# Kernel tuning notes

Hardware: AMD Instinct MI355X
Metric: run time of the kernel (lower is better)

Reference implementation:

```python
import jax, jax.numpy as jnp
import numpy as np

INPUT_DIM, ATTN_DIM, OUTPUT_DIM = 1024, 1024, 1024
B, LQ, LKV = 4, 2048, 2048


def setup_inputs() -> dict:
    key = jax.random.key(0)
    ks = jax.random.split(key, 10)
    s = 1.0 / np.sqrt(INPUT_DIM)
    return {
        "primary": jax.random.normal(ks[0], (B, LQ, INPUT_DIM), jnp.float32),
        "context_sequence": jax.random.normal(ks[1], (B, LKV, INPUT_DIM), jnp.float32),
        "mask": jax.random.randint(ks[2], (B, LQ, LKV), 0, 2).astype(jnp.float32),
        "Wq": jax.random.uniform(ks[3], (INPUT_DIM, ATTN_DIM), jnp.float32, -s, s),
        "bq": jax.random.uniform(ks[4], (ATTN_DIM,), jnp.float32, -s, s),
        "Wk": jax.random.uniform(ks[5], (INPUT_DIM, ATTN_DIM), jnp.float32, -s, s),
        "bk": jax.random.uniform(ks[6], (ATTN_DIM,), jnp.float32, -s, s),
        "Wv": jax.random.uniform(ks[7], (INPUT_DIM, OUTPUT_DIM), jnp.float32, -s, s),
        "bv": jax.random.uniform(ks[8], (OUTPUT_DIM,), jnp.float32, -s, s),
    }


def reference(primary, context_sequence, mask, Wq, bq, Wk, bk, Wv, bv):
    q = primary @ Wq + bq                      # [B, Lq, attn_dim]
    k = context_sequence @ Wk + bk             # [B, Lkv, attn_dim]
    v = context_sequence @ Wv + bv             # [B, Lkv, output_dim]
    score = jnp.einsum('bqd,bkd->bqk', q, k) / jnp.sqrt(jnp.float32(ATTN_DIM))
    score = score + mask * (-1e9)
    attn = jax.nn.softmax(score, axis=-1)
    return jnp.einsum('bqk,bkd->bqd', attn, v)  # [B, Lq, output_dim]
```

## Files before the change

### kernel.cpp

```cpp
#include <hip/hip_runtime.h>
#include <stdint.h>

typedef unsigned short u16;
typedef __bf16 bf16_t;
typedef bf16_t bf16x8 __attribute__((ext_vector_type(8)));
typedef float f32x4 __attribute__((ext_vector_type(4)));
typedef u16 u16x4 __attribute__((ext_vector_type(4)));
typedef u16 u16x8 __attribute__((ext_vector_type(8)));

__device__ __forceinline__ u16 f2bf(float f) {
  union { float f; uint32_t u; } v;
  v.f = f;
  uint32_t u = v.u + 0x7fffu + ((v.u >> 16) & 1u);
  return (u16)(u >> 16);
}

__device__ __forceinline__ float bf2f(u16 x) {
  union { uint32_t u; float f; } v;
  v.u = ((uint32_t)x) << 16;
  return v.f;
}

__device__ __forceinline__ void gload16(const void* g, void* l) {
  __builtin_amdgcn_global_load_lds(
      (__attribute__((address_space(1))) void*)g,
      (__attribute__((address_space(3))) void*)l, 16, 0, 0);
}

__device__ __forceinline__ f32x4 mfma16(bf16x8 a, bf16x8 b, f32x4 c) {
  return __builtin_amdgcn_mfma_f32_16x16x32_bf16(a, b, c, 0, 0, 0);
}

__global__ __launch_bounds__(256) void cvt_wt(
    const float* __restrict__ prim, u16* __restrict__ prim_bf,
    const float* __restrict__ ctx, u16* __restrict__ ctx_bf,
    const float* __restrict__ Wq, const float* __restrict__ Wk,
    const float* __restrict__ Wv, u16* __restrict__ Oq,
    u16* __restrict__ Ok, u16* __restrict__ Ov) {
  int b = blockIdx.x;
  if (b < 2048) {
    const float* in = (b < 1024) ? prim : ctx;
    u16* out = (b < 1024) ? prim_bf : ctx_bf;
    int bb = b & 1023;
    int i = bb * 256 + threadIdx.x;
    const int n4 = 2097152;
    for (; i < n4; i += 1024 * 256) {
      float4 v = *((const float4*)in + i);
      u16x4 o;
      o.x = f2bf(v.x); o.y = f2bf(v.y); o.z = f2bf(v.z); o.w = f2bf(v.w);
      *((u16x4*)out + i) = o;
    }
  } else {
    int tb = b - 2048;
    int zi = tb >> 10, rem = tb & 1023;
    const float* W = zi == 0 ? Wq : (zi == 1 ? Wk : Wv);
    u16* O = zi == 0 ? Oq : (zi == 1 ? Ok : Ov);
    __shared__ float t[32][33];
    int x = threadIdx.x & 31, y = threadIdx.x >> 5;
    int n0 = (rem & 31) * 32, k0 = (rem >> 5) * 32;
#pragma unroll
    for (int i = 0; i < 32; i += 8)
      t[y + i][x] = W[(size_t)(k0 + y + i) * 1024 + n0 + x];
    __syncthreads();
#pragma unroll
    for (int i = 0; i < 32; i += 8)
      O[(size_t)(n0 + y + i) * 1024 + k0 + x] = f2bf(t[x][y + i]);
  }
}

template <typename CT>
__device__ __forceinline__ void gemm_body(
    const u16* __restrict__ A, const u16* __restrict__ Bt,
    const float* __restrict__ biasCol, const float* __restrict__ biasRow,
    CT* __restrict__ C, int bm, int bn, int K, int lda, int ldb, int ldc) {
  __shared__ u16 aLds[2][256 * 64];
  __shared__ u16 bLds[2][256 * 64];
  int tid = threadIdx.x;
  int lane = tid & 63, w = tid >> 6;
  int l15 = lane & 15, g = lane >> 4;
  int wr = w >> 2, wc = w & 3;
  int NT = K >> 6;

  f32x4 acc[8][4] = {};

  auto stageA = [&](int buf, int h, int tk) {
    int k0 = tk * 64;
    int r = tid >> 3, cd = (tid & 7) * 8;
    int cs = cd ^ ((r & 7) * 8);
    int row0 = h * 64 + r;
    gload16(A + (size_t)(bm + row0) * lda + k0 + cs, &aLds[buf][row0 * 64 + cd]);
    int row1 = row0 + 128;
    gload16(A + (size_t)(bm + row1) * lda + k0 + cs, &aLds[buf][row1 * 64 + cd]);
  };
  auto stageB = [&](int buf, int x, int tk) {
    int k0 = tk * 64;
#pragma unroll
    for (int l = 0; l < 2; ++l) {
      int u = l * 512 + tid;
      int r = u >> 3, cd = (u & 7) * 8;
      int cs = cd ^ ((r & 7) * 8);
      int row = x * 128 + r;
      gload16(Bt + (size_t)(bn + row) * ldb + k0 + cs, &bLds[buf][row * 64 + cd]);
    }
  };
  auto ldA = [&](int buf, int m, int kc) -> bf16x8 {
    int row = wr * 128 + m * 16 + l15;
    int col = (kc * 32 + g * 8) ^ ((row & 7) * 8);
    return *(const bf16x8*)&aLds[buf][row * 64 + col];
  };
  auto ldB = [&](int buf, int j, int kc) -> bf16x8 {
    int row = wc * 64 + j * 16 + l15;
    int col = (kc * 32 + g * 8) ^ ((row & 7) * 8);
    return *(const bf16x8*)&bLds[buf][row * 64 + col];
  };

  stageA(0, 0, 0);
  stageB(0, 0, 0);
  stageB(0, 1, 0);
  stageA(0, 1, 0);
  int t1c = NT > 1 ? 1 : 0;
  stageA(1, 0, t1c);
  stageB(1, 0, t1c);
  asm volatile("s_waitcnt vmcnt(6)" ::: "memory");
  __builtin_amdgcn_s_barrier();

  for (int t = 0; t < NT; ++t) {
    int cur = t & 1, nxt = cur ^ 1;
    int tn1 = (t + 1 < NT) ? t + 1 : NT - 1;
    int tn2 = (t + 2 < NT) ? t + 2 : NT - 1;
    bf16x8 a0[4], b0[4], b1[4];

#pragma unroll
    for (int i = 0; i < 4; ++i) a0[i] = ldA(cur, i, 0);
#pragma unroll
    for (int j = 0; j < 4; ++j) b0[j] = ldB(cur, j, 0);
    stageB(nxt, 1, tn1);
    __builtin_amdgcn_s_barrier();
    asm volatile("s_waitcnt lgkmcnt(0)" ::: "memory");
    __builtin_amdgcn_sched_barrier(0);
    __builtin_amdgcn_s_setprio(1);
#pragma unroll
    for (int i = 0; i < 4; ++i)
#pragma unroll
      for (int j = 0; j < 4; ++j) acc[i][j] = mfma16(a0[i], b0[j], acc[i][j]);
    __builtin_amdgcn_s_setprio(0);
    __builtin_amdgcn_s_barrier();

#pragma unroll
    for (int i = 0; i < 4; ++i) a0[i] = ldA(cur, i, 1);
#pragma unroll
    for (int j = 0; j < 4; ++j) b1[j] = ldB(cur, j, 1);
    stageA(nxt, 1, tn1);
    __builtin_amdgcn_s_barrier();
    asm volatile("s_waitcnt lgkmcnt(0)" ::: "memory");
    __builtin_amdgcn_sched_barrier(0);
    __builtin_amdgcn_s_setprio(1);
#pragma unroll
    for (int i = 0; i < 4; ++i)
#pragma unroll
      for (int j = 0; j < 4; ++j) acc[i][j] = mfma16(a0[i], b1[j], acc[i][j]);
    __builtin_amdgcn_s_setprio(0);
    asm volatile("s_waitcnt vmcnt(8)" ::: "memory");
    __builtin_amdgcn_s_barrier();

#pragma unroll
    for (int i = 0; i < 4; ++i) a0[i] = ldA(cur, 4 + i, 0);
    stageA(cur, 0, tn2);
    __builtin_amdgcn_s_barrier();
    asm volatile("s_waitcnt lgkmcnt(0)" ::: "memory");
    __builtin_amdgcn_sched_barrier(0);
    __builtin_amdgcn_s_setprio(1);
#pragma unroll
    for (int i = 0; i < 4; ++i)
#pragma unroll
      for (int j = 0; j < 4; ++j) acc[4 + i][j] = mfma16(a0[i], b0[j], acc[4 + i][j]);
    __builtin_amdgcn_s_setprio(0);
    __builtin_amdgcn_s_barrier();

#pragma unroll
    for (int i = 0; i < 4; ++i) a0[i] = ldA(cur, 4 + i, 1);
    stageB(cur, 0, tn2);
    __builtin_amdgcn_s_barrier();
    asm volatile("s_waitcnt lgkmcnt(0)" ::: "memory");
    __builtin_amdgcn_sched_barrier(0);
    __builtin_amdgcn_s_setprio(1);
#pragma unroll
    for (int i = 0; i < 4; ++i)
#pragma unroll
      for (int j = 0; j < 4; ++j) acc[4 + i][j] = mfma16(a0[i], b1[j], acc[4 + i][j]);
    __builtin_amdgcn_s_setprio(0);
    asm volatile("s_waitcnt vmcnt(6)" ::: "memory");
    __builtin_amdgcn_s_barrier();
  }

#pragma unroll
  for (int mi = 0; mi < 8; ++mi) {
    int row = bm + wr * 128 + mi * 16 + g * 4;
#pragma unroll
    for (int j = 0; j < 4; ++j) {
      int col = bn + wc * 64 + j * 16 + l15;
      float bcv = biasCol ? biasCol[col] : 0.0f;
#pragma unroll
      for (int rr = 0; rr < 4; ++rr) {
        float brv = biasRow ? biasRow[row + rr] : 0.0f;
        float v = acc[mi][j][rr] + bcv + brv;
        if constexpr (sizeof(CT) == 2)
          C[(size_t)(row + rr) * ldc + col] = f2bf(v);
        else
          C[(size_t)(row + rr) * ldc + col] = v;
      }
    }
  }
}

__global__ __launch_bounds__(512, 2) void proj3(
    const u16* __restrict__ prim_ctx,
    const u16* __restrict__ wqk,
    const u16* __restrict__ wvt,
    const u16* __restrict__ ctx_bf,
    const float* __restrict__ bq, const float* __restrict__ bk,
    const float* __restrict__ bv,
    u16* __restrict__ qk,
    u16* __restrict__ vt) {
  int bz = blockIdx.z;
  if (bz < 2) {
    gemm_body<u16>(prim_ctx + (size_t)bz * 8192 * 1024,
                   wqk + (size_t)bz * 1024 * 1024,
                   bz ? bk : bq, nullptr,
                   qk + (size_t)bz * 8192 * 1024,
                   blockIdx.x * 256, blockIdx.y * 256, 1024, 1024, 1024, 1024);
  } else {
    int lin = blockIdx.x + 32 * blockIdx.y;
    int vx = lin & 3, vy = lin >> 2;
    gemm_body<u16>(wvt, ctx_bf, nullptr, bv, vt,
                   vx * 256, vy * 256, 1024, 1024, 1024, 8192);
  }
}

template <typename CT>
__global__ __launch_bounds__(512, 2) void gemm256(
    const u16* __restrict__ A, const u16* __restrict__ Bt,
    CT* __restrict__ C, int K, int lda, int ldb, int ldc,
    long long bsA, long long bsB, long long bsC) {
  gemm_body<CT>(A + (size_t)blockIdx.z * bsA, Bt + (size_t)blockIdx.z * bsB,
                nullptr, nullptr, C + (size_t)blockIdx.z * bsC,
                blockIdx.x * 256, blockIdx.y * 256, K, lda, ldb, ldc);
}

__global__ __launch_bounds__(256) void softmax_mask(
    const u16* __restrict__ S, const float* __restrict__ mask, u16* __restrict__ P) {
  const float C1 = 0.04508422f;
  const float C2 = -1.4426950e9f;
  int wid = (blockIdx.x * blockDim.x + threadIdx.x) >> 6;
  int lane = threadIdx.x & 63;
  size_t base = (size_t)wid * 2048;
  const u16* sp = S + base;
  const float* mp = mask + base;

  float a[32];
#pragma unroll
  for (int pass = 0; pass < 4; ++pass) {
    int e0 = pass * 512 + lane * 8;
    u16x8 sv = *(const u16x8*)(sp + e0);
    float4 m0 = *(const float4*)(mp + e0);
    float4 m1 = *(const float4*)(mp + e0 + 4);
    a[pass * 8 + 0] = bf2f(sv[0]) * C1 + m0.x * C2;
    a[pass * 8 + 1] = bf2f(sv[1]) * C1 + m0.y * C2;
    a[pass * 8 + 2] = bf2f(sv[2]) * C1 + m0.z * C2;
    a[pass * 8 + 3] = bf2f(sv[3]) * C1 + m0.w * C2;
    a[pass * 8 + 4] = bf2f(sv[4]) * C1 + m1.x * C2;
    a[pass * 8 + 5] = bf2f(sv[5]) * C1 + m1.y * C2;
    a[pass * 8 + 6] = bf2f(sv[6]) * C1 + m1.z * C2;
    a[pass * 8 + 7] = bf2f(sv[7]) * C1 + m1.w * C2;
  }
  float m = a[0];
#pragma unroll
  for (int i = 1; i < 32; ++i) m = fmaxf(m, a[i]);
#pragma unroll
  for (int off = 32; off >= 1; off >>= 1) m = fmaxf(m, __shfl_xor(m, off));

  float s = 0.0f;
#pragma unroll
  for (int i = 0; i < 32; ++i) {
    a[i] = exp2f(a[i] - m);
    s += a[i];
  }
#pragma unroll
  for (int off = 32; off >= 1; off >>= 1) s += __shfl_xor(s, off);
  float inv = 1.0f / s;

  u16* pp = P + base;
#pragma unroll
  for (int pass = 0; pass < 4; ++pass) {
    int e0 = pass * 512 + lane * 8;
    u16x8 o;
#pragma unroll
    for (int j = 0; j < 8; ++j) o[j] = f2bf(a[pass * 8 + j] * inv);
    *(u16x8*)(pp + e0) = o;
  }
}

extern "C" void kernel_launch(void* const* d_in, const int* in_sizes, int n_in,
                              void* d_out, int out_size, void* d_ws, size_t ws_size,
                              hipStream_t stream) {
  const float* primary = (const float*)d_in[0];
  const float* ctx     = (const float*)d_in[1];
  const float* mask    = (const float*)d_in[2];
  const float* Wq      = (const float*)d_in[3];
  const float* bq      = (const float*)d_in[4];
  const float* Wk      = (const float*)d_in[5];
  const float* bk      = (const float*)d_in[6];
  const float* Wv      = (const float*)d_in[7];
  const float* bv      = (const float*)d_in[8];
  float* out = (float*)d_out;

  char* ws = (char*)d_ws;
  u16* qbf     = (u16*)(ws);
  u16* kbf     = (u16*)(ws + 16777216);
  u16* vtbf    = (u16*)(ws + 2 * 16777216);
  u16* prim_bf = (u16*)(ws + 3 * 16777216);
  u16* ctx_bf  = (u16*)(ws + 4 * 16777216);
  u16* wqt     = (u16*)(ws + 5 * 16777216);
  u16* wkt     = (u16*)(ws + 5 * 16777216 + 2097152);
  u16* wvt     = (u16*)(ws + 5 * 16777216 + 2 * 2097152);
  u16* sbf     = (u16*)(ws + 3 * 16777216);
  u16* pbf     = (u16*)(ws);

  cvt_wt<<<5120, 256, 0, stream>>>(primary, prim_bf, ctx, ctx_bf,
                                   Wq, Wk, Wv, wqt, wkt, wvt);
  proj3<<<dim3(32, 4, 3), 512, 0, stream>>>(
      prim_bf, wqt, wvt, ctx_bf, bq, bk, bv, qbf, vtbf);
  gemm256<u16><<<dim3(8, 8, 4), 512, 0, stream>>>(
      qbf, kbf, sbf, 1024, 1024, 1024, 2048,
      2048 * 1024LL, 2048 * 1024LL, 2048 * 2048LL);
  softmax_mask<<<2048, 256, 0, stream>>>(sbf, mask, pbf);
  gemm256<float><<<dim3(8, 4, 4), 512, 0, stream>>>(
      pbf, vtbf, out, 2048, 2048, 8192, 1024,
      2048 * 2048LL, 2048LL, 2048 * 1024LL);
}
```

Baseline: 235.4 us.

## Reassociate QK^T through fused Wq·Wk^T matrix and drop K projection

The score matrix is rewritten as X·(Wq·Wk^T)·C^T plus a per-key bias vector C·(Wk·bq). Terms involving bk are constant along each softmax row, so they are dropped. A small 1024x1024 GEMM builds the fused matrix, a matvec builds the bias vector, and the softmax adds that vector to the scores. This removes the full K-projection GEMM over the context. In exchange it adds an extra launch whose GEMM part has only 16 blocks, extra bf16 rounding of the fused matrix, and a reshuffled workspace layout.

```diff
diff --git a/kernel.cpp b/kernel.cpp
--- a/kernel.cpp
+++ b/kernel.cpp
@@ -29,43 +29,6 @@
 
 __device__ __forceinline__ f32x4 mfma16(bf16x8 a, bf16x8 b, f32x4 c) {
   return __builtin_amdgcn_mfma_f32_16x16x32_bf16(a, b, c, 0, 0, 0);
-}
-
-__global__ __launch_bounds__(256) void cvt_wt(
-    const float* __restrict__ prim, u16* __restrict__ prim_bf,
-    const float* __restrict__ ctx, u16* __restrict__ ctx_bf,
-    const float* __restrict__ Wq, const float* __restrict__ Wk,
-    const float* __restrict__ Wv, u16* __restrict__ Oq,
-    u16* __restrict__ Ok, u16* __restrict__ Ov) {
-  int b = blockIdx.x;
-  if (b < 2048) {
-    const float* in = (b < 1024) ? prim : ctx;
-    u16* out = (b < 1024) ? prim_bf : ctx_bf;
-    int bb = b & 1023;
-    int i = bb * 256 + threadIdx.x;
-    const int n4 = 2097152;
-    for (; i < n4; i += 1024 * 256) {
-      float4 v = *((const float4*)in + i);
-      u16x4 o;
-      o.x = f2bf(v.x); o.y = f2bf(v.y); o.z = f2bf(v.z); o.w = f2bf(v.w);
-      *((u16x4*)out + i) = o;
-    }
-  } else {
-    int tb = b - 2048;
-    int zi = tb >> 10, rem = tb & 1023;
-    const float* W = zi == 0 ? Wq : (zi == 1 ? Wk : Wv);
-    u16* O = zi == 0 ? Oq : (zi == 1 ? Ok : Ov);
-    __shared__ float t[32][33];
-    int x = threadIdx.x & 31, y = threadIdx.x >> 5;
-    int n0 = (rem & 31) * 32, k0 = (rem >> 5) * 32;
-#pragma unroll
-    for (int i = 0; i < 32; i += 8)
-      t[y + i][x] = W[(size_t)(k0 + y + i) * 1024 + n0 + x];
-    __syncthreads();
-#pragma unroll
-    for (int i = 0; i < 32; i += 8)
-      O[(size_t)(n0 + y + i) * 1024 + k0 + x] = f2bf(t[x][y + i]);
-  }
 }
 
 template <typename CT>
@@ -213,49 +176,147 @@
   }
 }
 
-__global__ __launch_bounds__(512, 2) void proj3(
-    const u16* __restrict__ prim_ctx,
-    const u16* __restrict__ wqk,
-    const u16* __restrict__ wvt,
-    const u16* __restrict__ ctx_bf,
-    const float* __restrict__ bq, const float* __restrict__ bk,
-    const float* __restrict__ bv,
-    u16* __restrict__ qk,
-    u16* __restrict__ vt) {
-  int bz = blockIdx.z;
-  if (bz < 2) {
-    gemm_body<u16>(prim_ctx + (size_t)bz * 8192 * 1024,
-                   wqk + (size_t)bz * 1024 * 1024,
-                   bz ? bk : bq, nullptr,
-                   qk + (size_t)bz * 8192 * 1024,
+__global__ __launch_bounds__(256) void cvt_wt(
+    const float* __restrict__ prim, u16* __restrict__ prim_bf,
+    const float* __restrict__ ctx, u16* __restrict__ ctx_bf,
+    const float* __restrict__ Wq, const float* __restrict__ Wk,
+    const float* __restrict__ Wv, u16* __restrict__ Wq_bf,
+    u16* __restrict__ Wk_bf, u16* __restrict__ Ov,
+    const float* __restrict__ bq, float* __restrict__ wvec) {
+  int b = blockIdx.x;
+  if (b < 2048) {
+    const float* in = (b < 1024) ? prim : ctx;
+    u16* out = (b < 1024) ? prim_bf : ctx_bf;
+    int bb = b & 1023;
+    int i = bb * 256 + threadIdx.x;
+    const int n4 = 2097152;
+    for (; i < n4; i += 1024 * 256) {
+      float4 v = *((const float4*)in + i);
+      u16x4 o;
+      o.x = f2bf(v.x); o.y = f2bf(v.y); o.z = f2bf(v.z); o.w = f2bf(v.w);
+      *((u16x4*)out + i) = o;
+    }
+  } else if (b < 4096) {
+    const float* W = (b < 3072) ? Wq : Wk;
+    u16* O = (b < 3072) ? Wq_bf : Wk_bf;
+    int bb = (b - 2048) & 1023;
+    int i = bb * 256 + threadIdx.x;
+    float4 v = *((const float4*)W + i);
+    u16x4 o;
+    o.x = f2bf(v.x); o.y = f2bf(v.y); o.z = f2bf(v.z); o.w = f2bf(v.w);
+    *((u16x4*)O + i) = o;
+  } else if (b < 5120) {
+    int rem = b - 4096;
+    __shared__ float t[32][33];
+    int x = threadIdx.x & 31, y = threadIdx.x >> 5;
+    int n0 = (rem & 31) * 32, k0 = (rem >> 5) * 32;
+#pragma unroll
+    for (int i = 0; i < 32; i += 8)
+      t[y + i][x] = Wv[(size_t)(k0 + y + i) * 1024 + n0 + x];
+    __syncthreads();
+#pragma unroll
+    for (int i = 0; i < 32; i += 8)
+      Ov[(size_t)(n0 + y + i) * 1024 + k0 + x] = f2bf(t[x][y + i]);
+  } else {
+    int gw = (b - 5120) * 4 + (threadIdx.x >> 6);
+    int lane = threadIdx.x & 63;
+    for (int y = gw; y < 1024; y += 64) {
+      const float* row = Wk + (size_t)y * 1024 + lane * 16;
+      const float* bp = bq + lane * 16;
+      float s = 0.0f;
+#pragma unroll
+      for (int c = 0; c < 4; ++c) {
+        float4 a = *(const float4*)(row + c * 4);
+        float4 q = *(const float4*)(bp + c * 4);
+        s += a.x * q.x + a.y * q.y + a.z * q.z + a.w * q.w;
+      }
+#pragma unroll
+      for (int off = 32; off >= 1; off >>= 1) s += __shfl_xor(s, off);
+      if (lane == 0) wvec[y] = s;
+    }
+  }
+}
+
+__global__ __launch_bounds__(512, 2) void mt_v(
+    const u16* __restrict__ Wk_bf, const u16* __restrict__ Wq_bf,
+    u16* __restrict__ MT, const u16* __restrict__ ctx_bf,
+    const float* __restrict__ wvec, float* __restrict__ v) {
+  int b = blockIdx.x;
+  if (b < 16) {
+    gemm_body<u16>(Wk_bf, Wq_bf, nullptr, nullptr, MT,
+                   (b & 3) * 256, (b >> 2) * 256, 1024, 1024, 1024, 1024);
+  } else {
+    int gw = (b - 16) * 8 + (threadIdx.x >> 6);
+    int lane = threadIdx.x & 63;
+#pragma unroll
+    for (int r = 0; r < 8; ++r) {
+      int j = gw * 8 + r;
+      const u16* row = ctx_bf + (size_t)j * 1024 + lane * 16;
+      const float* wp = wvec + lane * 16;
+      u16x8 c0 = *(const u16x8*)row;
+      u16x8 c1 = *(const u16x8*)(row + 8);
+      float s = 0.0f;
+#pragma unroll
+      for (int e = 0; e < 8; ++e) s += bf2f(c0[e]) * wp[e];
+#pragma unroll
+      for (int e = 0; e < 8; ++e) s += bf2f(c1[e]) * wp[8 + e];
+#pragma unroll
+      for (int off = 32; off >= 1; off >>= 1) s += __shfl_xor(s, off);
+      if (lane == 0) v[j] = s;
+    }
+  }
+}
+
+__global__ __launch_bounds__(512, 2) void proj2(
+    const u16* __restrict__ prim_bf, const u16* __restrict__ MT,
+    const u16* __restrict__ wvt, const u16* __restrict__ ctx_bf,
+    const float* __restrict__ bv, u16* __restrict__ T, u16* __restrict__ vt) {
+  if (blockIdx.z == 0) {
+    gemm_body<u16>(prim_bf, MT, nullptr, nullptr, T,
                    blockIdx.x * 256, blockIdx.y * 256, 1024, 1024, 1024, 1024);
   } else {
     int lin = blockIdx.x + 32 * blockIdx.y;
-    int vx = lin & 3, vy = lin >> 2;
     gemm_body<u16>(wvt, ctx_bf, nullptr, bv, vt,
-                   vx * 256, vy * 256, 1024, 1024, 1024, 8192);
-  }
-}
-
-template <typename CT>
-__global__ __launch_bounds__(512, 2) void gemm256(
+                   (lin & 3) * 256, (lin >> 2) * 256, 1024, 1024, 1024, 8192);
+  }
+}
+
+__global__ __launch_bounds__(512, 2) void gemm_s(
     const u16* __restrict__ A, const u16* __restrict__ Bt,
-    CT* __restrict__ C, int K, int lda, int ldb, int ldc,
-    long long bsA, long long bsB, long long bsC) {
-  gemm_body<CT>(A + (size_t)blockIdx.z * bsA, Bt + (size_t)blockIdx.z * bsB,
-                nullptr, nullptr, C + (size_t)blockIdx.z * bsC,
-                blockIdx.x * 256, blockIdx.y * 256, K, lda, ldb, ldc);
+    u16* __restrict__ Clo, u16* __restrict__ Chi) {
+  int bz = blockIdx.z;
+  u16* C = (bz < 2) ? Clo + (size_t)bz * 2048 * 2048
+                    : Chi + (size_t)(bz - 2) * 2048 * 2048;
+  gemm_body<u16>(A + (size_t)bz * 2048 * 1024, Bt + (size_t)bz * 2048 * 1024,
+                 nullptr, nullptr, C, blockIdx.x * 256, blockIdx.y * 256,
+                 1024, 1024, 1024, 2048);
+}
+
+__global__ __launch_bounds__(512, 2) void gemm_pv(
+    const u16* __restrict__ Alo, const u16* __restrict__ Ahi,
+    const u16* __restrict__ Bt, float* __restrict__ C) {
+  int bz = blockIdx.z;
+  const u16* A = (bz < 2) ? Alo + (size_t)bz * 2048 * 2048
+                          : Ahi + (size_t)(bz - 2) * 2048 * 2048;
+  gemm_body<float>(A, Bt + (size_t)bz * 2048, nullptr, nullptr,
+                   C + (size_t)bz * 2048 * 1024, blockIdx.x * 256,
+                   blockIdx.y * 256, 2048, 2048, 8192, 1024);
 }
 
 __global__ __launch_bounds__(256) void softmax_mask(
-    const u16* __restrict__ S, const float* __restrict__ mask, u16* __restrict__ P) {
+    const u16* __restrict__ Slo, const u16* __restrict__ Shi,
+    const float* __restrict__ mask, const float* __restrict__ v,
+    u16* __restrict__ Plo, u16* __restrict__ Phi) {
   const float C1 = 0.04508422f;
   const float C2 = -1.4426950e9f;
   int wid = (blockIdx.x * blockDim.x + threadIdx.x) >> 6;
   int lane = threadIdx.x & 63;
-  size_t base = (size_t)wid * 2048;
-  const u16* sp = S + base;
-  const float* mp = mask + base;
+  const u16* sp = (wid < 4096) ? Slo + (size_t)wid * 2048
+                               : Shi + (size_t)(wid - 4096) * 2048;
+  u16* pp = (wid < 4096) ? Plo + (size_t)wid * 2048
+                         : Phi + (size_t)(wid - 4096) * 2048;
+  const float* mp = mask + (size_t)wid * 2048;
+  const float* vp = v + (size_t)(wid >> 11) * 2048;
 
   float a[32];
 #pragma unroll
@@ -264,14 +325,16 @@
     u16x8 sv = *(const u16x8*)(sp + e0);
     float4 m0 = *(const float4*)(mp + e0);
     float4 m1 = *(const float4*)(mp + e0 + 4);
-    a[pass * 8 + 0] = bf2f(sv[0]) * C1 + m0.x * C2;
-    a[pass * 8 + 1] = bf2f(sv[1]) * C1 + m0.y * C2;
-    a[pass * 8 + 2] = bf2f(sv[2]) * C1 + m0.z * C2;
-    a[pass * 8 + 3] = bf2f(sv[3]) * C1 + m0.w * C2;
-    a[pass * 8 + 4] = bf2f(sv[4]) * C1 + m1.x * C2;
-    a[pass * 8 + 5] = bf2f(sv[5]) * C1 + m1.y * C2;
-    a[pass * 8 + 6] = bf2f(sv[6]) * C1 + m1.z * C2;
-    a[pass * 8 + 7] = bf2f(sv[7]) * C1 + m1.w * C2;
+    float4 v0 = *(const float4*)(vp + e0);
+    float4 v1 = *(const float4*)(vp + e0 + 4);
+    a[pass * 8 + 0] = (bf2f(sv[0]) + v0.x) * C1 + m0.x * C2;
+    a[pass * 8 + 1] = (bf2f(sv[1]) + v0.y) * C1 + m0.y * C2;
+    a[pass * 8 + 2] = (bf2f(sv[2]) + v0.z) * C1 + m0.z * C2;
+    a[pass * 8 + 3] = (bf2f(sv[3]) + v0.w) * C1 + m0.w * C2;
+    a[pass * 8 + 4] = (bf2f(sv[4]) + v1.x) * C1 + m1.x * C2;
+    a[pass * 8 + 5] = (bf2f(sv[5]) + v1.y) * C1 + m1.y * C2;
+    a[pass * 8 + 6] = (bf2f(sv[6]) + v1.z) * C1 + m1.z * C2;
+    a[pass * 8 + 7] = (bf2f(sv[7]) + v1.w) * C1 + m1.w * C2;
   }
   float m = a[0];
 #pragma unroll
@@ -289,7 +352,6 @@
   for (int off = 32; off >= 1; off >>= 1) s += __shfl_xor(s, off);
   float inv = 1.0f / s;
 
-  u16* pp = P + base;
 #pragma unroll
   for (int pass = 0; pass < 4; ++pass) {
     int e0 = pass * 512 + lane * 8;
@@ -313,28 +375,31 @@
   const float* Wv      = (const float*)d_in[7];
   const float* bv      = (const float*)d_in[8];
   float* out = (float*)d_out;
+  (void)bk;
 
   char* ws = (char*)d_ws;
-  u16* qbf     = (u16*)(ws);
-  u16* kbf     = (u16*)(ws + 16777216);
-  u16* vtbf    = (u16*)(ws + 2 * 16777216);
-  u16* prim_bf = (u16*)(ws + 3 * 16777216);
-  u16* ctx_bf  = (u16*)(ws + 4 * 16777216);
-  u16* wqt     = (u16*)(ws + 5 * 16777216);
-  u16* wkt     = (u16*)(ws + 5 * 16777216 + 2097152);
-  u16* wvt     = (u16*)(ws + 5 * 16777216 + 2 * 2097152);
-  u16* sbf     = (u16*)(ws + 3 * 16777216);
-  u16* pbf     = (u16*)(ws);
-
-  cvt_wt<<<5120, 256, 0, stream>>>(primary, prim_bf, ctx, ctx_bf,
-                                   Wq, Wk, Wv, wqt, wkt, wvt);
-  proj3<<<dim3(32, 4, 3), 512, 0, stream>>>(
-      prim_bf, wqt, wvt, ctx_bf, bq, bk, bv, qbf, vtbf);
-  gemm256<u16><<<dim3(8, 8, 4), 512, 0, stream>>>(
-      qbf, kbf, sbf, 1024, 1024, 1024, 2048,
-      2048 * 1024LL, 2048 * 1024LL, 2048 * 2048LL);
-  softmax_mask<<<2048, 256, 0, stream>>>(sbf, mask, pbf);
-  gemm256<float><<<dim3(8, 4, 4), 512, 0, stream>>>(
-      pbf, vtbf, out, 2048, 2048, 8192, 1024,
-      2048 * 2048LL, 2048LL, 2048 * 1024LL);
-}
+  u16* prim_bf = (u16*)(ws);
+  u16* ctx_bf  = (u16*)(ws + 16777216);
+  u16* vtbf    = (u16*)(ws + 33554432);
+  u16* Tbuf    = (u16*)(ws + 50331648);
+  u16* Wq_bf   = (u16*)(ws + 67108864);
+  u16* Wk_bf   = (u16*)(ws + 69206016);
+  u16* wvt     = (u16*)(ws + 83886080);
+  u16* MT      = (u16*)(ws + 85983232);
+  float* wvec  = (float*)(ws + 88080384);
+  float* vvec  = (float*)(ws + 88084480);
+  u16* sbf_lo  = (u16*)(ws);
+  u16* sbf_hi  = (u16*)(ws + 67108864);
+  u16* pbf_lo  = (u16*)(ws + 16777216);
+  u16* pbf_hi  = (u16*)(ws + 50331648);
+
+  cvt_wt<<<5136, 256, 0, stream>>>(primary, prim_bf, ctx, ctx_bf,
+                                   Wq, Wk, Wv, Wq_bf, Wk_bf, wvt, bq, wvec);
+  mt_v<<<144, 512, 0, stream>>>(Wk_bf, Wq_bf, MT, ctx_bf, wvec, vvec);
+  proj2<<<dim3(32, 4, 2), 512, 0, stream>>>(prim_bf, MT, wvt, ctx_bf, bv,
+                                            Tbuf, vtbf);
+  gemm_s<<<dim3(8, 8, 4), 512, 0, stream>>>(Tbuf, ctx_bf, sbf_lo, sbf_hi);
+  softmax_mask<<<2048, 256, 0, stream>>>(sbf_lo, sbf_hi, mask, vvec,
+                                         pbf_lo, pbf_hi);
+  gemm_pv<<<dim3(8, 4, 4), 512, 0, stream>>>(pbf_lo, pbf_hi, vtbf, out);
+}
```

Result: slower. 243.5 us (+3.4%).

## Store Q and K projections as FP8 and compute QK^T with FP8 MFMA

Applied to the files above, without the earlier changes.

The Q/K projection epilogue now writes FP8 (e4m3) values instead of bf16, and a new dedicated FP8 GEMM kernel computes the score matrix using 16x16x32 fp8 MFMA with byte-sized LDS tiles. Shared memory buffers are hoisted out of gemm_body so different kernels can supply their own. This halves the bytes moved for Q/K and uses the higher-throughput FP8 matrix path for the score GEMM, at the cost of reduced precision in the scores, which then feed a softmax over large-magnitude values.

```diff
diff --git a/kernel.cpp b/kernel.cpp
--- a/kernel.cpp
+++ b/kernel.cpp
@@ -2,6 +2,7 @@
 #include <stdint.h>
 
 typedef unsigned short u16;
+typedef unsigned char u8;
 typedef __bf16 bf16_t;
 typedef bf16_t bf16x8 __attribute__((ext_vector_type(8)));
 typedef float f32x4 __attribute__((ext_vector_type(4)));
@@ -70,11 +71,10 @@
 
 template <typename CT>
 __device__ __forceinline__ void gemm_body(
+    u16* aL, u16* bL,
     const u16* __restrict__ A, const u16* __restrict__ Bt,
     const float* __restrict__ biasCol, const float* __restrict__ biasRow,
     CT* __restrict__ C, int bm, int bn, int K, int lda, int ldb, int ldc) {
-  __shared__ u16 aLds[2][256 * 64];
-  __shared__ u16 bLds[2][256 * 64];
   int tid = threadIdx.x;
   int lane = tid & 63, w = tid >> 6;
   int l15 = lane & 15, g = lane >> 4;
@@ -88,9 +88,9 @@
     int r = tid >> 3, cd = (tid & 7) * 8;
     int cs = cd ^ ((r & 7) * 8);
     int row0 = h * 64 + r;
-    gload16(A + (size_t)(bm + row0) * lda + k0 + cs, &aLds[buf][row0 * 64 + cd]);
+    gload16(A + (size_t)(bm + row0) * lda + k0 + cs, aL + buf * 16384 + row0 * 64 + cd);
     int row1 = row0 + 128;
-    gload16(A + (size_t)(bm + row1) * lda + k0 + cs, &aLds[buf][row1 * 64 + cd]);
+    gload16(A + (size_t)(bm + row1) * lda + k0 + cs, aL + buf * 16384 + row1 * 64 + cd);
   };
   auto stageB = [&](int buf, int x, int tk) {
     int k0 = tk * 64;
@@ -100,18 +100,18 @@
       int r = u >> 3, cd = (u & 7) * 8;
       int cs = cd ^ ((r & 7) * 8);
       int row = x * 128 + r;
-      gload16(Bt + (size_t)(bn + row) * ldb + k0 + cs, &bLds[buf][row * 64 + cd]);
+      gload16(Bt + (size_t)(bn + row) * ldb + k0 + cs, bL + buf * 16384 + row * 64 + cd);
     }
   };
   auto ldA = [&](int buf, int m, int kc) -> bf16x8 {
     int row = wr * 128 + m * 16 + l15;
     int col = (kc * 32 + g * 8) ^ ((row & 7) * 8);
-    return *(const bf16x8*)&aLds[buf][row * 64 + col];
+    return *(const bf16x8*)(aL + buf * 16384 + row * 64 + col);
   };
   auto ldB = [&](int buf, int j, int kc) -> bf16x8 {
     int row = wc * 64 + j * 16 + l15;
     int col = (kc * 32 + g * 8) ^ ((row & 7) * 8);
-    return *(const bf16x8*)&bLds[buf][row * 64 + col];
+    return *(const bf16x8*)(bL + buf * 16384 + row * 64 + col);
   };
 
   stageA(0, 0, 0);
@@ -204,36 +204,180 @@
       for (int rr = 0; rr < 4; ++rr) {
         float brv = biasRow ? biasRow[row + rr] : 0.0f;
         float v = acc[mi][j][rr] + bcv + brv;
-        if constexpr (sizeof(CT) == 2)
+        if constexpr (sizeof(CT) == 1) {
+          unsigned int p = __builtin_amdgcn_cvt_pk_fp8_f32(v, v, 0, false);
+          C[(size_t)(row + rr) * ldc + col] = (CT)(p & 0xff);
+        } else if constexpr (sizeof(CT) == 2) {
           C[(size_t)(row + rr) * ldc + col] = f2bf(v);
-        else
+        } else {
           C[(size_t)(row + rr) * ldc + col] = v;
+        }
       }
     }
   }
 }
 
 __global__ __launch_bounds__(512, 2) void proj3(
-    const u16* __restrict__ prim_ctx,
-    const u16* __restrict__ wqk,
-    const u16* __restrict__ wvt,
-    const u16* __restrict__ ctx_bf,
+    const u16* __restrict__ prim_ctx, const u16* __restrict__ wqk,
+    const u16* __restrict__ wvt, const u16* __restrict__ ctx_bf,
     const float* __restrict__ bq, const float* __restrict__ bk,
     const float* __restrict__ bv,
-    u16* __restrict__ qk,
-    u16* __restrict__ vt) {
+    u8* __restrict__ qk8, u16* __restrict__ vt) {
+  __shared__ u16 smem[4 * 16384];
+  u16* aL = smem;
+  u16* bL = smem + 2 * 16384;
   int bz = blockIdx.z;
   if (bz < 2) {
-    gemm_body<u16>(prim_ctx + (size_t)bz * 8192 * 1024,
-                   wqk + (size_t)bz * 1024 * 1024,
-                   bz ? bk : bq, nullptr,
-                   qk + (size_t)bz * 8192 * 1024,
-                   blockIdx.x * 256, blockIdx.y * 256, 1024, 1024, 1024, 1024);
+    gemm_body<u8>(aL, bL,
+                  prim_ctx + (size_t)bz * 8192 * 1024,
+                  wqk + (size_t)bz * 1024 * 1024,
+                  bz ? bk : bq, nullptr,
+                  qk8 + (size_t)bz * 8192 * 1024,
+                  blockIdx.x * 256, blockIdx.y * 256, 1024, 1024, 1024, 1024);
   } else {
     int lin = blockIdx.x + 32 * blockIdx.y;
-    int vx = lin & 3, vy = lin >> 2;
-    gemm_body<u16>(wvt, ctx_bf, nullptr, bv, vt,
-                   vx * 256, vy * 256, 1024, 1024, 1024, 8192);
+    gemm_body<u16>(aL, bL, wvt, ctx_bf, nullptr, bv, vt,
+                   (lin & 3) * 256, (lin >> 2) * 256, 1024, 1024, 1024, 8192);
+  }
+}
+
+__global__ __launch_bounds__(512, 2) void gemm_s8(
+    const u8* __restrict__ A, const u8* __restrict__ Bt, u16* __restrict__ C) {
+  const int lda = 1024, ldb = 1024, ldc = 2048, K = 1024;
+  const u8* Ab = A + (size_t)blockIdx.z * 2048 * 1024;
+  const u8* Bb = Bt + (size_t)blockIdx.z * 2048 * 1024;
+  u16* Cb = C + (size_t)blockIdx.z * 2048 * 2048;
+  int bm = blockIdx.x * 256, bn = blockIdx.y * 256;
+
+  __shared__ u8 aLds[2][256 * 64];
+  __shared__ u8 bLds[2][256 * 64];
+  int tid = threadIdx.x;
+  int lane = tid & 63, w = tid >> 6;
+  int l15 = lane & 15, g = lane >> 4;
+  int wr = w >> 2, wc = w & 3;
+  int NT = K >> 6;
+
+  f32x4 acc[8][4] = {};
+
+  auto stageA = [&](int buf, int h, int tk) {
+    int k0 = tk * 64;
+    int r = tid >> 2;
+    int row = h * 64 + (r & 63) + (r >> 6) * 128;
+    int cd = (tid & 3) * 16;
+    int cs = cd ^ ((row & 3) * 16);
+    gload16(Ab + (size_t)(bm + row) * lda + k0 + cs, &aLds[buf][row * 64 + cd]);
+  };
+  auto stageB = [&](int buf, int x, int tk) {
+    int k0 = tk * 64;
+    int row = x * 128 + (tid >> 2);
+    int cd = (tid & 3) * 16;
+    int cs = cd ^ ((row & 3) * 16);
+    gload16(Bb + (size_t)(bn + row) * ldb + k0 + cs, &bLds[buf][row * 64 + cd]);
+  };
+  auto ldA = [&](int buf, int m, int kc) -> long {
+    int row = wr * 128 + m * 16 + l15;
+    int colb = (kc * 32 + g * 8) ^ ((row & 3) * 16);
+    return *(const long*)&aLds[buf][row * 64 + colb];
+  };
+  auto ldB = [&](int buf, int j, int kc) -> long {
+    int row = wc * 64 + j * 16 + l15;
+    int colb = (kc * 32 + g * 8) ^ ((row & 3) * 16);
+    return *(const long*)&bLds[buf][row * 64 + colb];
+  };
+
+  stageA(0, 0, 0);
+  stageB(0, 0, 0);
+  stageB(0, 1, 0);
+  stageA(0, 1, 0);
+  int t1c = NT > 1 ? 1 : 0;
+  stageA(1, 0, t1c);
+  stageB(1, 0, t1c);
+  asm volatile("s_waitcnt vmcnt(3)" ::: "memory");
+  __builtin_amdgcn_s_barrier();
+
+  for (int t = 0; t < NT; ++t) {
+    int cur = t & 1, nxt = cur ^ 1;
+    int tn1 = (t + 1 < NT) ? t + 1 : NT - 1;
+    int tn2 = (t + 2 < NT) ? t + 2 : NT - 1;
+    long a0[4], b0[4], b1[4];
+
+#pragma unroll
+    for (int i = 0; i < 4; ++i) a0[i] = ldA(cur, i, 0);
+#pragma unroll
+    for (int j = 0; j < 4; ++j) b0[j] = ldB(cur, j, 0);
+    stageB(nxt, 1, tn1);
+    __builtin_amdgcn_s_barrier();
+    asm volatile("s_waitcnt lgkmcnt(0)" ::: "memory");
+    __builtin_amdgcn_sched_barrier(0);
+    __builtin_amdgcn_s_setprio(1);
+#pragma unroll
+    for (int i = 0; i < 4; ++i)
+#pragma unroll
+      for (int j = 0; j < 4; ++j)
+        acc[i][j] = __builtin_amdgcn_mfma_f32_16x16x32_fp8_fp8(a0[i], b0[j], acc[i][j], 0, 0, 0);
+    __builtin_amdgcn_s_setprio(0);
+    __builtin_amdgcn_s_barrier();
+
+#pragma unroll
+    for (int i = 0; i < 4; ++i) a0[i] = ldA(cur, i, 1);
+#pragma unroll
+    for (int j = 0; j < 4; ++j) b1[j] = ldB(cur, j, 1);
+    stageA(nxt, 1, tn1);
+    __builtin_amdgcn_s_barrier();
+    asm volatile("s_waitcnt lgkmcnt(0)" ::: "memory");
+    __builtin_amdgcn_sched_barrier(0);
+    __builtin_amdgcn_s_setprio(1);
+#pragma unroll
+    for (int i = 0; i < 4; ++i)
+#pragma unroll
+      for (int j = 0; j < 4; ++j)
+        acc[i][j] = __builtin_amdgcn_mfma_f32_16x16x32_fp8_fp8(a0[i], b1[j], acc[i][j], 0, 0, 0);
+    __builtin_amdgcn_s_setprio(0);
+    asm volatile("s_waitcnt vmcnt(4)" ::: "memory");
+    __builtin_amdgcn_s_barrier();
+
+#pragma unroll
+    for (int i = 0; i < 4; ++i) a0[i] = ldA(cur, 4 + i, 0);
+    stageA(cur, 0, tn2);
+    __builtin_amdgcn_s_barrier();
+    asm volatile("s_waitcnt lgkmcnt(0)" ::: "memory");
+    __builtin_amdgcn_sched_barrier(0);
+    __builtin_amdgcn_s_setprio(1);
+#pragma unroll
+    for (int i = 0; i < 4; ++i)
+#pragma unroll
+      for (int j = 0; j < 4; ++j)
+        acc[4 + i][j] = __builtin_amdgcn_mfma_f32_16x16x32_fp8_fp8(a0[i], b0[j], acc[4 + i][j], 0, 0, 0);
+    __builtin_amdgcn_s_setprio(0);
+    __builtin_amdgcn_s_barrier();
+
+#pragma unroll
+    for (int i = 0; i < 4; ++i) a0[i] = ldA(cur, 4 + i, 1);
+    stageB(cur, 0, tn2);
+    __builtin_amdgcn_s_barrier();
+    asm volatile("s_waitcnt lgkmcnt(0)" ::: "memory");
+    __builtin_amdgcn_sched_barrier(0);
+    __builtin_amdgcn_s_setprio(1);
+#pragma unroll
+    for (int i = 0; i < 4; ++i)
+#pragma unroll
+      for (int j = 0; j < 4; ++j)
+        acc[4 + i][j] = __builtin_amdgcn_mfma_f32_16x16x32_fp8_fp8(a0[i], b1[j], acc[4 + i][j], 0, 0, 0);
+    __builtin_amdgcn_s_setprio(0);
+    asm volatile("s_waitcnt vmcnt(3)" ::: "memory");
+    __builtin_amdgcn_s_barrier();
+  }
+
+#pragma unroll
+  for (int mi = 0; mi < 8; ++mi) {
+    int row = bm + wr * 128 + mi * 16 + g * 4;
+#pragma unroll
+    for (int j = 0; j < 4; ++j) {
+      int col = bn + wc * 64 + j * 16 + l15;
+#pragma unroll
+      for (int rr = 0; rr < 4; ++rr)
+        Cb[(size_t)(row + rr) * ldc + col] = f2bf(acc[mi][j][rr]);
+    }
   }
 }
 
@@ -242,7 +386,9 @@
     const u16* __restrict__ A, const u16* __restrict__ Bt,
     CT* __restrict__ C, int K, int lda, int ldb, int ldc,
     long long bsA, long long bsB, long long bsC) {
-  gemm_body<CT>(A + (size_t)blockIdx.z * bsA, Bt + (size_t)blockIdx.z * bsB,
+  __shared__ u16 smem[4 * 16384];
+  gemm_body<CT>(smem, smem + 2 * 16384,
+                A + (size_t)blockIdx.z * bsA, Bt + (size_t)blockIdx.z * bsB,
                 nullptr, nullptr, C + (size_t)blockIdx.z * bsC,
                 blockIdx.x * 256, blockIdx.y * 256, K, lda, ldb, ldc);
 }
@@ -315,8 +461,7 @@
   float* out = (float*)d_out;
 
   char* ws = (char*)d_ws;
-  u16* qbf     = (u16*)(ws);
-  u16* kbf     = (u16*)(ws + 16777216);
+  u8*  qk8     = (u8*)(ws);
   u16* vtbf    = (u16*)(ws + 2 * 16777216);
   u16* prim_bf = (u16*)(ws + 3 * 16777216);
   u16* ctx_bf  = (u16*)(ws + 4 * 16777216);
@@ -329,10 +474,8 @@
   cvt_wt<<<5120, 256, 0, stream>>>(primary, prim_bf, ctx, ctx_bf,
                                    Wq, Wk, Wv, wqt, wkt, wvt);
   proj3<<<dim3(32, 4, 3), 512, 0, stream>>>(
-      prim_bf, wqt, wvt, ctx_bf, bq, bk, bv, qbf, vtbf);
-  gemm256<u16><<<dim3(8, 8, 4), 512, 0, stream>>>(
-      qbf, kbf, sbf, 1024, 1024, 1024, 2048,
-      2048 * 1024LL, 2048 * 1024LL, 2048 * 2048LL);
+      prim_bf, wqt, wvt, ctx_bf, bq, bk, bv, qk8, vtbf);
+  gemm_s8<<<dim3(8, 8, 4), 512, 0, stream>>>(qk8, qk8 + 8192 * 1024, sbf);
   softmax_mask<<<2048, 256, 0, stream>>>(sbf, mask, pbf);
   gemm256<float><<<dim3(8, 4, 4), 512, 0, stream>>>(
       pbf, vtbf, out, 2048, 2048, 8192, 1024,
```

Measured after the change: 219.8 us. 1.07x faster.
